# Optimization experiments

Hardware: AMD Instinct MI355X
Metric: run time of the kernel (lower is better)

The kernel has to match this reference:

```python
import jax, jax.numpy as jnp
import numpy as np

D_MODEL = 1024
NUM_HEADS = 16
GROUP_SIZE = 4
NUM_GROUPS = NUM_HEADS // GROUP_SIZE  # 4
D_K = D_MODEL // NUM_HEADS            # 64
THETA = 10000.0
WINDOW = 512


def _rope(x, positions):
    # x: (..., t, d) with d even; interleaved-pair rotation, freq_i = theta^{-i/(d/2)}
    d = x.shape[-1]
    half = d // 2
    inv_freq = THETA ** (-jnp.arange(half, dtype=x.dtype) / half)          # (half,)
    ang = positions.astype(x.dtype)[:, None] * inv_freq[None, :]           # (t, half)
    cos, sin = jnp.cos(ang), jnp.sin(ang)
    x1, x2 = x[..., 0::2], x[..., 1::2]
    r1 = x1 * cos - x2 * sin
    r2 = x1 * sin + x2 * cos
    return jnp.stack([r1, r2], axis=-1).reshape(x.shape)


def setup_inputs() -> dict:
    key = jax.random.key(0)
    k1, k2, k3, k4, k5 = jax.random.split(key, 5)
    b, t = 2, 2048
    scale = 1.0 / np.sqrt(D_MODEL)
    return {
        "x": jax.random.normal(k1, (b, t, D_MODEL), dtype=jnp.float32),
        "WQ": jax.random.normal(k2, (D_MODEL, D_MODEL), dtype=jnp.float32) * scale,
        "WK": jax.random.normal(k3, (NUM_GROUPS * D_K, D_MODEL), dtype=jnp.float32) * scale,
        "WV": jax.random.normal(k4, (NUM_GROUPS * D_K, D_MODEL), dtype=jnp.float32) * scale,
        "WO": jax.random.normal(k5, (D_MODEL, D_MODEL), dtype=jnp.float32) * scale,
        "token_positions": jnp.arange(t, dtype=jnp.int32),
    }


def reference(x, WQ, WK, WV, WO, token_positions):
    b, t, _ = x.shape
    g, s, d = NUM_GROUPS, GROUP_SIZE, D_K
    # projections (Linear: y = x @ W^T, no bias)
    q = (x @ WQ.T).reshape(b, t, g, s, d).transpose(0, 2, 3, 1, 4)  # b g s t d
    k = (x @ WK.T).reshape(b, t, g, d).transpose(0, 2, 1, 3)        # b g t d
    v = (x @ WV.T).reshape(b, t, g, d).transpose(0, 2, 1, 3)        # b g t d
    q = _rope(q, token_positions)
    k = _rope(k, token_positions)
    # scores: kv heads shared across the s query heads of each group
    scores = jnp.einsum('bgsqd,bgkd->bgsqk', q, k) / jnp.sqrt(jnp.asarray(d, x.dtype))
    i = jnp.arange(t)[:, None]
    j = jnp.arange(t)[None, :]
    allowed = (i >= j) & (i - j <= WINDOW)  # causal sliding window
    scores = jnp.where(allowed, scores, -jnp.inf)
    probs = jax.nn.softmax(scores, axis=-1)
    out = jnp.einsum('bgsqk,bgkd->bgsqd', probs, v)                 # b g s t d
    out = out.transpose(0, 3, 1, 2, 4).reshape(b, t, D_MODEL)       # b t (g s d)
    return out @ WO.T
```

## Files before the change

### kernel.cpp

```cpp
#include <hip/hip_runtime.h>
#include <hip/hip_bf16.h>

typedef __bf16 bf16;
typedef __bf16 bf16x4 __attribute__((ext_vector_type(4)));
typedef __bf16 bf16x8 __attribute__((ext_vector_type(8)));
typedef float  floatx4 __attribute__((ext_vector_type(4)));

#define D_MODEL   1024
#define NUM_HEADS 16
#define NUM_GROUPS 4
#define DK        64
#define SEQ_T     2048
#define BATCH     2
#define M_ROWS    (BATCH*SEQ_T)
#define WINDOW    512
#define KV_DIM    (NUM_GROUPS*DK)
#define N_QKV     (D_MODEL + 2*KV_DIM)
#define QSCALE    0.1803368801111204f
#define FREQ_C    0.4152410118609203f

#define GLDS16(g, l)                                                          \
    __builtin_amdgcn_global_load_lds(                                         \
        (const __attribute__((address_space(1))) void*)(g),                   \
        (__attribute__((address_space(3))) void*)(l), 16, 0, 0)

__global__ __launch_bounds__(256)
void convert_all(const float* s0, bf16* d0, int c0,
                 const float* s1, bf16* d1, int c1,
                 const float* s2, bf16* d2, int c2,
                 const float* s3, bf16* d3, int c3,
                 const float* s4, bf16* d4, int c4)
{
    int id = blockIdx.x * 256 + threadIdx.x;
    const float* src; bf16* dst;
    if      (id < c0)         { src = s0; dst = d0; }
    else if ((id -= c0) < c1) { src = s1; dst = d1; }
    else if ((id -= c1) < c2) { src = s2; dst = d2; }
    else if ((id -= c2) < c3) { src = s3; dst = d3; }
    else if ((id -= c3) < c4) { src = s4; dst = d4; }
    else return;
    int i = id * 8;
    const float* s = src + i;
    float4 a = *(const float4*)s;
    float4 b = *(const float4*)(s + 4);
    bf16x8 v;
    v[0] = (bf16)a.x; v[1] = (bf16)a.y; v[2] = (bf16)a.z; v[3] = (bf16)a.w;
    v[4] = (bf16)b.x; v[5] = (bf16)b.y; v[6] = (bf16)b.z; v[7] = (bf16)b.w;
    *(bf16x8*)&dst[i] = v;
}

__global__ __launch_bounds__(256, 3)
void gemm_t64(const bf16* __restrict__ A, const bf16* __restrict__ W, int K,
              bf16* __restrict__ Cq, bf16* __restrict__ Ck, bf16* __restrict__ Vt,
              float* __restrict__ Co, const int* __restrict__ pos, int mode)
{
    __shared__ bf16 As[2][128 * 64];
    __shared__ bf16 Bs[2][64 * 64];

    const int tid  = threadIdx.x;
    const int wave = tid >> 6;
    const int lane = tid & 63;
    const int lr   = lane & 15;
    const int quad = lane >> 4;

    const int nx    = (mode == 0) ? (N_QKV / 64) : (D_MODEL / 64);
    const int bid   = blockIdx.x;
    const int chunk = gridDim.x >> 3;
    const int v     = (bid & 7) * chunk + (bid >> 3);
    const int m0    = (v / nx) * 128;
    const int n0    = (v % nx) * 64;

    const int wm = (wave >> 1) * 64;
    const int wn = (wave & 1) * 32;

    const int cr8 = lane >> 3;
    const int cc  = ((lane & 7) ^ cr8) * 8;
    const bf16* Ag = &A[(size_t)(m0 + cr8) * K + cc];
    const bf16* Wg = &W[(size_t)(n0 + cr8) * K + cc];

#define STAGE(buf, kk)                                                        \
    do {                                                                      \
        GLDS16(Ag + (size_t)((wave * 4 + 0) * 8) * K + (kk), &As[buf][(wave * 4 + 0) * 512]); \
        GLDS16(Ag + (size_t)((wave * 4 + 1) * 8) * K + (kk), &As[buf][(wave * 4 + 1) * 512]); \
        GLDS16(Ag + (size_t)((wave * 4 + 2) * 8) * K + (kk), &As[buf][(wave * 4 + 2) * 512]); \
        GLDS16(Ag + (size_t)((wave * 4 + 3) * 8) * K + (kk), &As[buf][(wave * 4 + 3) * 512]); \
        GLDS16(Wg + (size_t)((wave * 2 + 0) * 8) * K + (kk), &Bs[buf][(wave * 2 + 0) * 512]); \
        GLDS16(Wg + (size_t)((wave * 2 + 1) * 8) * K + (kk), &Bs[buf][(wave * 2 + 1) * 512]); \
    } while (0)

    const int ax0 = (quad ^ (lane & 7)) * 8;
    const int ax1 = ax0 ^ 32;

    floatx4 acc[4][2];
#pragma unroll
    for (int i = 0; i < 4; i++)
#pragma unroll
        for (int j = 0; j < 2; j++) acc[i][j] = (floatx4)(0.0f);

    STAGE(0, 0);

    int cur = 0;
    for (int k0 = 0; k0 < K; k0 += 64) {
        if (k0 + 64 < K) {
            STAGE(cur ^ 1, k0 + 64);
            __asm__ volatile("s_waitcnt vmcnt(6)" ::: "memory");
        } else {
            __asm__ volatile("s_waitcnt vmcnt(0)" ::: "memory");
        }
        __builtin_amdgcn_s_barrier();

        bf16x8 a0[4], a1[4], b0[2], b1[2];
#pragma unroll
        for (int mi = 0; mi < 4; mi++) {
            a0[mi] = *(const bf16x8*)&As[cur][(wm + mi * 16 + lr) * 64 + ax0];
            a1[mi] = *(const bf16x8*)&As[cur][(wm + mi * 16 + lr) * 64 + ax1];
        }
#pragma unroll
        for (int ni = 0; ni < 2; ni++) {
            b0[ni] = *(const bf16x8*)&Bs[cur][(wn + ni * 16 + lr) * 64 + ax0];
            b1[ni] = *(const bf16x8*)&Bs[cur][(wn + ni * 16 + lr) * 64 + ax1];
        }

#pragma unroll
        for (int mi = 0; mi < 4; mi++)
#pragma unroll
            for (int ni = 0; ni < 2; ni++) {
                acc[mi][ni] = __builtin_amdgcn_mfma_f32_16x16x32_bf16(
                    a0[mi], b0[ni], acc[mi][ni], 0, 0, 0);
                acc[mi][ni] = __builtin_amdgcn_mfma_f32_16x16x32_bf16(
                    a1[mi], b1[ni], acc[mi][ni], 0, 0, 0);
            }

        __builtin_amdgcn_s_barrier();
        cur ^= 1;
    }
#undef STAGE

    if (mode == 0) {
        if (n0 >= D_MODEL + KV_DIM) {
            const int g  = (n0 - (D_MODEL + KV_DIM)) >> 6;
            const int b  = m0 >> 11;
            const int bg = b * 4 + g;
#pragma unroll
            for (int mi = 0; mi < 4; mi++) {
#pragma unroll
                for (int ni = 0; ni < 2; ni++) {
                    int d  = wn + ni * 16 + lr;
                    int t0 = (m0 & (SEQ_T - 1)) + wm + mi * 16 + quad * 4;
                    bf16x4 vv;
#pragma unroll
                    for (int r = 0; r < 4; r++) vv[r] = (bf16)acc[mi][ni][r];
                    *(bf16x4*)&Vt[((size_t)(bg * 64 + d)) * SEQ_T + t0] = vv;
                }
            }
        } else {
            bf16* out; int ld, coff; float sc;
            if (n0 < D_MODEL) { out = Cq; ld = D_MODEL; coff = n0; sc = QSCALE; }
            else              { out = Ck; ld = KV_DIM;  coff = n0 - D_MODEL; sc = 1.0f; }
            float inv[2];
            float sgn = (lr & 1) ? 1.0f : -1.0f;
#pragma unroll
            for (int ni = 0; ni < 2; ni++) {
                int ip = (wn + ni * 16 + lr) >> 1;
                inv[ni] = exp2f(-(float)ip * FREQ_C);
            }
#pragma unroll
            for (int mi = 0; mi < 4; mi++) {
#pragma unroll
                for (int r = 0; r < 4; r++) {
                    int row = m0 + wm + mi * 16 + quad * 4 + r;
                    float p = (float)pos[row & (SEQ_T - 1)];
#pragma unroll
                    for (int ni = 0; ni < 2; ni++) {
                        float vv = acc[mi][ni][r];
                        float vp = __shfl_xor(vv, 1);
                        float ang = p * inv[ni];
                        float ss, cc2;
                        __sincosf(ang, &ss, &cc2);
                        vv = vv * cc2 + vp * ss * sgn;
                        out[(size_t)row * ld + coff + wn + ni * 16 + lr] = (bf16)(vv * sc);
                    }
                }
            }
        }
    } else {
#pragma unroll
        for (int mi = 0; mi < 4; mi++)
#pragma unroll
            for (int ni = 0; ni < 2; ni++)
#pragma unroll
                for (int r = 0; r < 4; r++) {
                    int row = m0 + wm + mi * 16 + quad * 4 + r;
                    int col = n0 + wn + ni * 16 + lr;
                    Co[(size_t)row * D_MODEL + col] = acc[mi][ni][r];
                }
    }
}

__global__ __launch_bounds__(256)
void attn_mfma(const bf16* __restrict__ Q, const bf16* __restrict__ K,
               const bf16* __restrict__ Vt_g, bf16* __restrict__ AO)
{
    const int ST = 72;
    __shared__ bf16 Ks[64 * ST];
    __shared__ bf16 Vt[80 * ST];
    __shared__ bf16 Ps[4 * 32 * ST];

    const int tid  = threadIdx.x;
    const int wave = tid >> 6;
    const int lane = tid & 63;
    const int lr   = lane & 15;
    const int quad = lane >> 4;
    const int bg = blockIdx.y;
    const int b = bg >> 2, g = bg & 3;
    const int h = g * 4 + wave;
    const int q0 = blockIdx.x * 32;

    bf16x8 qf[2][2];
#pragma unroll
    for (int mi = 0; mi < 2; mi++)
#pragma unroll
        for (int ks = 0; ks < 2; ks++)
            qf[mi][ks] = *(const bf16x8*)
                &Q[((size_t)(b * SEQ_T + q0 + mi * 16 + lr)) * D_MODEL
                   + h * 64 + ks * 32 + quad * 8];

    for (int i = tid; i < 15 * ST; i += 256) Vt[65 * ST + i] = (bf16)0.0f;
    if (tid < ST) Vt[64 * ST + tid] = (bf16)(tid < 64 ? 1.0f : 0.0f);

    bf16* Pw = &Ps[wave * 32 * ST];

    floatx4 o[2][5];
#pragma unroll
    for (int mi = 0; mi < 2; mi++)
#pragma unroll
        for (int nt = 0; nt < 5; nt++) o[mi][nt] = (floatx4)(0.0f);

    const int t0   = (q0 >= WINDOW) ? ((q0 - WINDOW) & ~63) : 0;
    const int last = q0 & ~63;

    const int srow0 = tid >> 3,         scol0 = (tid & 7) * 8;
    const int srow1 = (tid + 256) >> 3, scol1 = ((tid + 256) & 7) * 8;

    bf16x8 kreg[2], vreg[2];
#define LOADKV(jn)                                                            \
    do {                                                                      \
        kreg[0] = *(const bf16x8*)&K[((size_t)(b * SEQ_T + (jn) + srow0)) * KV_DIM + g * 64 + scol0]; \
        vreg[0] = *(const bf16x8*)&Vt_g[((size_t)(bg * 64 + srow0)) * SEQ_T + (jn) + scol0];          \
        kreg[1] = *(const bf16x8*)&K[((size_t)(b * SEQ_T + (jn) + srow1)) * KV_DIM + g * 64 + scol1]; \
        vreg[1] = *(const bf16x8*)&Vt_g[((size_t)(bg * 64 + srow1)) * SEQ_T + (jn) + scol1];          \
    } while (0)

    LOADKV(t0);

    for (int j0 = t0; j0 <= last; j0 += 64) {
        const bool mC = (j0 == last);
        const bool mW = (q0 >= WINDOW) && (j0 == t0);
        __syncthreads();
        *(bf16x8*)&Ks[srow0 * ST + scol0] = kreg[0];
        *(bf16x8*)&Vt[srow0 * ST + scol0] = vreg[0];
        *(bf16x8*)&Ks[srow1 * ST + scol1] = kreg[1];
        *(bf16x8*)&Vt[srow1 * ST + scol1] = vreg[1];
        if (j0 + 64 <= last) LOADKV(j0 + 64);
        __syncthreads();

        floatx4 s[2][4];
#pragma unroll
        for (int mi = 0; mi < 2; mi++)
#pragma unroll
            for (int nt = 0; nt < 4; nt++) s[mi][nt] = (floatx4)(0.0f);
#pragma unroll
        for (int ks = 0; ks < 2; ks++) {
#pragma unroll
            for (int nt = 0; nt < 4; nt++) {
                bf16x8 kf = *(const bf16x8*)&Ks[(nt * 16 + lr) * ST + ks * 32 + quad * 8];
                s[0][nt] = __builtin_amdgcn_mfma_f32_16x16x32_bf16(qf[0][ks], kf, s[0][nt], 0, 0, 0);
                s[1][nt] = __builtin_amdgcn_mfma_f32_16x16x32_bf16(qf[1][ks], kf, s[1][nt], 0, 0, 0);
            }
        }

        if (mC) {
#pragma unroll
            for (int mi = 0; mi < 2; mi++)
#pragma unroll
                for (int nt = 0; nt < 4; nt++) {
                    int key = j0 + nt * 16 + lr;
#pragma unroll
                    for (int r = 0; r < 4; r++) {
                        int qi_ = q0 + mi * 16 + quad * 4 + r;
                        s[mi][nt][r] = (key <= qi_) ? s[mi][nt][r] : -1e30f;
                    }
                }
        } else if (mW) {
#pragma unroll
            for (int mi = 0; mi < 2; mi++)
#pragma unroll
                for (int nt = 0; nt < 4; nt++) {
                    int key = j0 + nt * 16 + lr;
#pragma unroll
                    for (int r = 0; r < 4; r++) {
                        int qi_ = q0 + mi * 16 + quad * 4 + r;
                        s[mi][nt][r] = (qi_ - key <= WINDOW) ? s[mi][nt][r] : -1e30f;
                    }
                }
        }

#pragma unroll
        for (int mi = 0; mi < 2; mi++)
#pragma unroll
            for (int nt = 0; nt < 4; nt++)
#pragma unroll
                for (int r = 0; r < 4; r++)
                    Pw[(mi * 16 + quad * 4 + r) * ST + nt * 16 + lr] =
                        (bf16)exp2f(s[mi][nt][r]);

        __asm__ volatile("s_waitcnt lgkmcnt(0)" ::: "memory");

#pragma unroll
        for (int ks = 0; ks < 2; ks++) {
            bf16x8 pf0 = *(const bf16x8*)&Pw[(0 + lr) * ST + ks * 32 + quad * 8];
            bf16x8 pf1 = *(const bf16x8*)&Pw[(16 + lr) * ST + ks * 32 + quad * 8];
#pragma unroll
            for (int nt = 0; nt < 5; nt++) {
                bf16x8 vf = *(const bf16x8*)&Vt[(nt * 16 + lr) * ST + ks * 32 + quad * 8];
                o[0][nt] = __builtin_amdgcn_mfma_f32_16x16x32_bf16(pf0, vf, o[0][nt], 0, 0, 0);
                o[1][nt] = __builtin_amdgcn_mfma_f32_16x16x32_bf16(pf1, vf, o[1][nt], 0, 0, 0);
            }
        }
    }
#undef LOADKV

#pragma unroll
    for (int mi = 0; mi < 2; mi++)
#pragma unroll
        for (int r = 0; r < 4; r++) {
            float l = __shfl(o[mi][4][r], lane & 48);
            float invl = 1.0f / l;
            int row = q0 + mi * 16 + quad * 4 + r;
#pragma unroll
            for (int nt = 0; nt < 4; nt++)
                AO[((size_t)(b * SEQ_T + row)) * D_MODEL + h * 64 + nt * 16 + lr] =
                    (bf16)(o[mi][nt][r] * invl);
        }
}

extern "C" void kernel_launch(void* const* d_in, const int* in_sizes, int n_in,
                              void* d_out, int out_size, void* d_ws, size_t ws_size,
                              hipStream_t stream)
{
    const float* x  = (const float*)d_in[0];
    const float* WQ = (const float*)d_in[1];
    const float* WK = (const float*)d_in[2];
    const float* WV = (const float*)d_in[3];
    const float* WO = (const float*)d_in[4];
    const int*  pos = (const int*)d_in[5];

    char* ws   = (char*)d_ws;
    bf16* Qw   = (bf16*)ws;
    bf16* Kw   = (bf16*)(ws + (size_t) 8 * 1024 * 1024);
    bf16* Vt_g = (bf16*)(ws + (size_t)10 * 1024 * 1024);
    bf16* xb   = (bf16*)(ws + (size_t)12 * 1024 * 1024);
    bf16* AO   = xb;
    bf16* Wqkv = (bf16*)(ws + (size_t)20 * 1024 * 1024);
    bf16* WOb  = (bf16*)(ws + (size_t)23 * 1024 * 1024);

    const int cx = (M_ROWS * D_MODEL) / 8;
    const int cq = (D_MODEL * D_MODEL) / 8;
    const int ck = (KV_DIM * D_MODEL) / 8;
    const int ctot = cx + cq + 2 * ck + cq;
    convert_all<<<ctot / 256, 256, 0, stream>>>(
        x, xb, cx,
        WQ, Wqkv, cq,
        WK, Wqkv + (size_t)D_MODEL * D_MODEL, ck,
        WV, Wqkv + (size_t)(D_MODEL + KV_DIM) * D_MODEL, ck,
        WO, WOb, cq);

    gemm_t64<<<(N_QKV / 64) * (M_ROWS / 128), 256, 0, stream>>>(
        xb, Wqkv, D_MODEL, Qw, Kw, Vt_g, nullptr, pos, 0);

    attn_mfma<<<dim3(SEQ_T / 32, BATCH * NUM_GROUPS), 256, 0, stream>>>(
        Qw, Kw, Vt_g, AO);

    gemm_t64<<<(D_MODEL / 64) * (M_ROWS / 128), 256, 0, stream>>>(
        AO, WOb, D_MODEL, nullptr, nullptr, nullptr, (float*)d_out, pos, 1);
}
```

Measured before the change: 141.2 us.

## Keep attention probabilities in registers by transposing QK^T and permuting V layout

Swaps the MFMA operand order so the score tile comes out transposed (keys along rows). Each lane can then pack its exp2 results directly into the bf16x8 A-operand of the PV MFMA. To match that register order, V is stored into LDS with a permuted column layout. This removes the per-wave P scratch buffer in LDS, its stores, the waitcnt and the reloads, which also lowers LDS usage per block. The cost is a more intricate index permutation that must line up exactly with the MFMA register layout.

```diff
diff --git a/kernel.cpp b/kernel.cpp
--- a/kernel.cpp
+++ b/kernel.cpp
@@ -204,7 +204,6 @@
     const int ST = 72;
     __shared__ bf16 Ks[64 * ST];
     __shared__ bf16 Vt[80 * ST];
-    __shared__ bf16 Ps[4 * 32 * ST];
 
     const int tid  = threadIdx.x;
     const int wave = tid >> 6;
@@ -228,8 +227,6 @@
     for (int i = tid; i < 15 * ST; i += 256) Vt[65 * ST + i] = (bf16)0.0f;
     if (tid < ST) Vt[64 * ST + tid] = (bf16)(tid < 64 ? 1.0f : 0.0f);
 
-    bf16* Pw = &Ps[wave * 32 * ST];
-
     floatx4 o[2][5];
 #pragma unroll
     for (int mi = 0; mi < 2; mi++)
@@ -241,6 +238,11 @@
 
     const int srow0 = tid >> 3,         scol0 = (tid & 7) * 8;
     const int srow1 = (tid + 256) >> 3, scol1 = ((tid + 256) & 7) * 8;
+
+    const int wc0 = scol0 & 31;
+    const int w00 = (scol0 & ~31) + ((wc0 & 15) >> 2) * 8 + (wc0 >> 4) * 4;
+    const int wc1 = scol1 & 31;
+    const int w10 = (scol1 & ~31) + ((wc1 & 15) >> 2) * 8 + (wc1 >> 4) * 4;
 
     bf16x8 kreg[2], vreg[2];
 #define LOADKV(jn)                                                            \
@@ -258,73 +260,77 @@
         const bool mW = (q0 >= WINDOW) && (j0 == t0);
         __syncthreads();
         *(bf16x8*)&Ks[srow0 * ST + scol0] = kreg[0];
-        *(bf16x8*)&Vt[srow0 * ST + scol0] = vreg[0];
         *(bf16x8*)&Ks[srow1 * ST + scol1] = kreg[1];
-        *(bf16x8*)&Vt[srow1 * ST + scol1] = vreg[1];
+        *(bf16x4*)&Vt[srow0 * ST + w00] =
+            __builtin_shufflevector(vreg[0], vreg[0], 0, 1, 2, 3);
+        *(bf16x4*)&Vt[srow0 * ST + w00 + 8] =
+            __builtin_shufflevector(vreg[0], vreg[0], 4, 5, 6, 7);
+        *(bf16x4*)&Vt[srow1 * ST + w10] =
+            __builtin_shufflevector(vreg[1], vreg[1], 0, 1, 2, 3);
+        *(bf16x4*)&Vt[srow1 * ST + w10 + 8] =
+            __builtin_shufflevector(vreg[1], vreg[1], 4, 5, 6, 7);
         if (j0 + 64 <= last) LOADKV(j0 + 64);
         __syncthreads();
 
-        floatx4 s[2][4];
-#pragma unroll
-        for (int mi = 0; mi < 2; mi++)
-#pragma unroll
-            for (int nt = 0; nt < 4; nt++) s[mi][nt] = (floatx4)(0.0f);
+        floatx4 s2[4][2];
+#pragma unroll
+        for (int nt = 0; nt < 4; nt++)
+#pragma unroll
+            for (int mi = 0; mi < 2; mi++) s2[nt][mi] = (floatx4)(0.0f);
 #pragma unroll
         for (int ks = 0; ks < 2; ks++) {
 #pragma unroll
             for (int nt = 0; nt < 4; nt++) {
                 bf16x8 kf = *(const bf16x8*)&Ks[(nt * 16 + lr) * ST + ks * 32 + quad * 8];
-                s[0][nt] = __builtin_amdgcn_mfma_f32_16x16x32_bf16(qf[0][ks], kf, s[0][nt], 0, 0, 0);
-                s[1][nt] = __builtin_amdgcn_mfma_f32_16x16x32_bf16(qf[1][ks], kf, s[1][nt], 0, 0, 0);
+                s2[nt][0] = __builtin_amdgcn_mfma_f32_16x16x32_bf16(kf, qf[0][ks], s2[nt][0], 0, 0, 0);
+                s2[nt][1] = __builtin_amdgcn_mfma_f32_16x16x32_bf16(kf, qf[1][ks], s2[nt][1], 0, 0, 0);
             }
         }
 
         if (mC) {
 #pragma unroll
-            for (int mi = 0; mi < 2; mi++)
-#pragma unroll
-                for (int nt = 0; nt < 4; nt++) {
-                    int key = j0 + nt * 16 + lr;
+            for (int nt = 0; nt < 4; nt++)
+#pragma unroll
+                for (int mi = 0; mi < 2; mi++) {
+                    int qi_ = q0 + mi * 16 + lr;
 #pragma unroll
                     for (int r = 0; r < 4; r++) {
-                        int qi_ = q0 + mi * 16 + quad * 4 + r;
-                        s[mi][nt][r] = (key <= qi_) ? s[mi][nt][r] : -1e30f;
+                        int key = j0 + nt * 16 + quad * 4 + r;
+                        s2[nt][mi][r] = (key <= qi_) ? s2[nt][mi][r] : -1e30f;
                     }
                 }
         } else if (mW) {
 #pragma unroll
-            for (int mi = 0; mi < 2; mi++)
-#pragma unroll
-                for (int nt = 0; nt < 4; nt++) {
-                    int key = j0 + nt * 16 + lr;
+            for (int nt = 0; nt < 4; nt++)
+#pragma unroll
+                for (int mi = 0; mi < 2; mi++) {
+                    int qi_ = q0 + mi * 16 + lr;
 #pragma unroll
                     for (int r = 0; r < 4; r++) {
-                        int qi_ = q0 + mi * 16 + quad * 4 + r;
-                        s[mi][nt][r] = (qi_ - key <= WINDOW) ? s[mi][nt][r] : -1e30f;
+                        int key = j0 + nt * 16 + quad * 4 + r;
+                        s2[nt][mi][r] = (qi_ - key <= WINDOW) ? s2[nt][mi][r] : -1e30f;
                     }
                 }
         }
 
+        bf16x8 pa[2][2];
 #pragma unroll
         for (int mi = 0; mi < 2; mi++)
 #pragma unroll
-            for (int nt = 0; nt < 4; nt++)
-#pragma unroll
-                for (int r = 0; r < 4; r++)
-                    Pw[(mi * 16 + quad * 4 + r) * ST + nt * 16 + lr] =
-                        (bf16)exp2f(s[mi][nt][r]);
-
-        __asm__ volatile("s_waitcnt lgkmcnt(0)" ::: "memory");
+            for (int ks = 0; ks < 2; ks++)
+#pragma unroll
+                for (int r = 0; r < 4; r++) {
+                    pa[mi][ks][r]     = (bf16)exp2f(s2[2 * ks][mi][r]);
+                    pa[mi][ks][r + 4] = (bf16)exp2f(s2[2 * ks + 1][mi][r]);
+                }
 
 #pragma unroll
         for (int ks = 0; ks < 2; ks++) {
-            bf16x8 pf0 = *(const bf16x8*)&Pw[(0 + lr) * ST + ks * 32 + quad * 8];
-            bf16x8 pf1 = *(const bf16x8*)&Pw[(16 + lr) * ST + ks * 32 + quad * 8];
 #pragma unroll
             for (int nt = 0; nt < 5; nt++) {
                 bf16x8 vf = *(const bf16x8*)&Vt[(nt * 16 + lr) * ST + ks * 32 + quad * 8];
-                o[0][nt] = __builtin_amdgcn_mfma_f32_16x16x32_bf16(pf0, vf, o[0][nt], 0, 0, 0);
-                o[1][nt] = __builtin_amdgcn_mfma_f32_16x16x32_bf16(pf1, vf, o[1][nt], 0, 0, 0);
+                o[0][nt] = __builtin_amdgcn_mfma_f32_16x16x32_bf16(pa[0][ks], vf, o[0][nt], 0, 0, 0);
+                o[1][nt] = __builtin_amdgcn_mfma_f32_16x16x32_bf16(pa[1][ks], vf, o[1][nt], 0, 0, 0);
             }
         }
     }
```

New measurement: 139.8 us. No clear change (-1.0%).
